# Optimization experiments

Hardware: AMD Instinct MI355X
Metric: run time of the kernel (lower is better)

The kernel has to match this reference:

```python
import jax, jax.numpy as jnp
import numpy as np

# token markers (module-level constants in the original repo)
PASS, MAP_EVT, STEP_EVT = 1, 2, 3
NUM_KEYS, NUM_VALUES, D_MODEL = 32, 32, 64
NUM_SYMBOLS = NUM_KEYS * 2  # 64
GRAPH_STEPS = 3
B, T = 4096, 256


def _mlp2(x, W1, b1, W2, b2):
    # Linear -> GELU (exact, matching torch nn.GELU default) -> Linear
    return jax.nn.gelu(x @ W1 + b1, approximate=False) @ W2 + b2


def setup_inputs() -> dict:
    key = jax.random.key(0)
    ks = jax.random.split(key, 32)
    d = D_MODEL

    def w(k, shape, scale=0.05):
        return jax.random.normal(k, shape, dtype=jnp.float32) * scale

    inp = {
        "evidence": jax.random.normal(ks[0], (B, T, d), dtype=jnp.float32),
        "event_marker": jax.random.randint(ks[1], (B, T), 0, 4, dtype=jnp.int32),
        "source_idx": jax.random.randint(ks[2], (B, T), 0, NUM_SYMBOLS, dtype=jnp.int32),
        "source_valid": jax.random.randint(ks[3], (B, T), 0, 2, dtype=jnp.int32),
        "target_symbol_idx": jax.random.randint(ks[4], (B, T), 0, NUM_SYMBOLS, dtype=jnp.int32),
        "target_symbol_valid": jax.random.randint(ks[5], (B, T), 0, 2, dtype=jnp.int32),
        "target_value_idx": jax.random.randint(ks[6], (B, T), 0, NUM_VALUES, dtype=jnp.int32),
        "target_value_valid": jax.random.randint(ks[7], (B, T), 0, 2, dtype=jnp.int32),
        "query_idx": jax.random.randint(ks[8], (B,), 0, NUM_SYMBOLS, dtype=jnp.int32),
        "query_valid": jax.random.randint(ks[9], (B,), 0, 2, dtype=jnp.int32),
        # embeddings
        "symbol_emb": w(ks[10], (NUM_SYMBOLS, d), 0.05),
        "value_emb": w(ks[11], (NUM_VALUES, d), 0.05),
        # map_gain MLP: Linear(d,d) GELU Linear(d,1)
        "mg_W1": w(ks[12], (d, d)), "mg_b1": jnp.zeros((d,), jnp.float32),
        "mg_W2": w(ks[13], (d, 1)), "mg_b2": jnp.zeros((1,), jnp.float32),
        # step_gain MLP
        "sg_W1": w(ks[14], (d, d)), "sg_b1": jnp.zeros((d,), jnp.float32),
        "sg_W2": w(ks[15], (d, 1)), "sg_b2": jnp.zeros((1,), jnp.float32),
        # slot_feedback MLP: Linear(2d,d) GELU Linear(d,d)
        "sf_W1": w(ks[16], (2 * d, d)), "sf_b1": jnp.zeros((d,), jnp.float32),
        "sf_W2": w(ks[17], (d, d)), "sf_b2": jnp.zeros((d,), jnp.float32),
        # output_head MLP: Linear(2d,d) GELU Linear(d,NUM_VALUES)
        "oh_W1": w(ks[18], (2 * d, d)), "oh_b1": jnp.zeros((d,), jnp.float32),
        "oh_W2": w(ks[19], (d, NUM_VALUES)), "oh_b2": jnp.zeros((NUM_VALUES,), jnp.float32),
    }
    return inp


def reference(evidence, event_marker, source_idx, source_valid, target_symbol_idx,
              target_symbol_valid, target_value_idx, target_value_valid,
              query_idx, query_valid, symbol_emb, value_emb,
              mg_W1, mg_b1, mg_W2, mg_b2, sg_W1, sg_b1, sg_W2, sg_b2,
              sf_W1, sf_b1, sf_W2, sf_b2, oh_W1, oh_b1, oh_W2, oh_b2):
    b, t = event_marker.shape
    dt = evidence.dtype

    # --- per-event gates (batched over all T events at once) ---
    map_gain = jax.nn.sigmoid(_mlp2(evidence, mg_W1, mg_b1, mg_W2, mg_b2))[..., 0]   # [B,T]
    step_gain = jax.nn.sigmoid(_mlp2(evidence, sg_W1, sg_b1, sg_W2, sg_b2))[..., 0]  # [B,T]

    src_v = source_valid.astype(bool)
    map_mask = ((event_marker == PASS) | (event_marker == MAP_EVT)) & src_v & target_value_valid.astype(bool)
    step_mask = (event_marker == STEP_EVT) & src_v & target_symbol_valid.astype(bool)

    src = jnp.clip(source_idx, 0, NUM_SYMBOLS - 1)
    tsym = jnp.clip(target_symbol_idx, 0, NUM_SYMBOLS - 1)
    tval = jnp.clip(target_value_idx, 0, NUM_VALUES - 1)

    # --- memory writes: sequential additive outer-product updates from a zero
    # init_state are order-independent, so they reduce to one scatter-add ---
    bb = jnp.broadcast_to(jnp.arange(b)[:, None], (b, t))
    map_memory = jnp.zeros((b, NUM_SYMBOLS, NUM_VALUES), dt).at[bb, src, tval].add(
        map_gain * map_mask.astype(dt))
    step_memory = jnp.zeros((b, NUM_SYMBOLS, NUM_SYMBOLS), dt).at[bb, src, tsym].add(
        step_gain * step_mask.astype(dt))

    # --- query_readout: 3-step graph walk ---
    walk = jax.nn.one_hot(jnp.clip(query_idx, 0, NUM_SYMBOLS - 1), NUM_SYMBOLS, dtype=dt)
    walk = walk * query_valid.astype(dt)[:, None]  # [B,S]

    acc_values = jnp.einsum('bs,bsv->bv', walk, map_memory)    # [B,V]
    acc_symbols = walk @ symbol_emb                             # [B,D]
    for _ in range(GRAPH_STEPS):
        walk = jnp.einsum('bs,bst->bt', walk, step_memory)
        acc_values = acc_values + jnp.einsum('bs,bsv->bv', walk, map_memory)
        acc_symbols = acc_symbols + walk @ symbol_emb

    graph_value_vec = acc_values @ value_emb                    # [B,D]
    graph_state = jnp.concatenate([acc_symbols, graph_value_vec], axis=-1)  # [B,2D]
    logits = _mlp2(graph_state, oh_W1, oh_b1, oh_W2, oh_b2)     # [B,NUM_VALUES]
    feedback = _mlp2(graph_state, sf_W1, sf_b1, sf_W2, sf_b2)   # [B,D]
    return logits, feedback
```

## Files before the change

### kernel.cpp

```cpp
#include <hip/hip_runtime.h>
#include <hip/hip_bf16.h>
#include <math.h>

#define T_LEN 256
#define NSYM 64
#define NVAL 32
#define DMOD 64

__device__ __forceinline__ float gelu_exact(float x) {
    return 0.5f * x * (1.0f + erff(x * 0.70710678118654752440f));
}
__device__ __forceinline__ float sigmoid_f(float x) {
    return 1.0f / (1.0f + expf(-x));
}

__global__ __launch_bounds__(256, 2) void k1_fused(
    const float* __restrict__ evidence,
    const int* __restrict__ event_marker,
    const int* __restrict__ source_idx,
    const int* __restrict__ source_valid,
    const int* __restrict__ tsym_idx,
    const int* __restrict__ tsym_valid,
    const int* __restrict__ tval_idx,
    const int* __restrict__ tval_valid,
    const int* __restrict__ query_idx,
    const int* __restrict__ query_valid,
    const float* __restrict__ symbol_emb,
    const float* __restrict__ value_emb,
    const float* __restrict__ mg_W1, const float* __restrict__ mg_b1,
    const float* __restrict__ mg_W2, const float* __restrict__ mg_b2,
    const float* __restrict__ sg_W1, const float* __restrict__ sg_b1,
    const float* __restrict__ sg_W2, const float* __restrict__ sg_b2,
    float* __restrict__ state_out)
{
    __shared__ int   s_src[T_LEN], s_tv[T_LEN], s_ts[T_LEN];
    __shared__ int   list_map[T_LEN], list_step[T_LEN];
    __shared__ int   cnts[2];
    __shared__ float mapM[NSYM * NVAL];
    __shared__ float stepM[NSYM * NSYM];
    __shared__ float W1s[64 * 64];
    __shared__ float W2s[64], b1s[64];
    __shared__ float b2s;
    __shared__ float X[64 * 65];
    __shared__ float wk[64], wk2[64], accv[32], accs[64];

    const int tid = threadIdx.x;
    const int b   = blockIdx.x;

    if (tid < 2) cnts[tid] = 0;
    for (int i = tid; i < NSYM * NVAL;  i += 256) mapM[i]  = 0.f;
    for (int i = tid; i < NSYM * NSYM;  i += 256) stepM[i] = 0.f;
    __syncthreads();

    {
        const int e  = b * T_LEN + tid;
        const int m  = event_marker[e];
        const int sv = source_valid[e];
        int src = source_idx[e]; src = src < 0 ? 0 : (src > 63 ? 63 : src);
        int ts  = tsym_idx[e];   ts  = ts  < 0 ? 0 : (ts  > 63 ? 63 : ts);
        int tv  = tval_idx[e];   tv  = tv  < 0 ? 0 : (tv  > 31 ? 31 : tv);
        s_src[tid] = src; s_ts[tid] = ts; s_tv[tid] = tv;
        const bool mm = ((m == 1) || (m == 2)) && (sv != 0) && (tval_valid[e] != 0);
        const bool sm = (m == 3) && (sv != 0) && (tsym_valid[e] != 0);
        if (mm) { int i = atomicAdd(&cnts[0], 1); list_map[i]  = tid; }
        if (sm) { int i = atomicAdd(&cnts[1], 1); list_step[i] = tid; }
    }
    __syncthreads();

    for (int type = 0; type < 2; ++type) {
        const float* W1g = (type == 0) ? mg_W1 : sg_W1;
        const float* W2g = (type == 0) ? mg_W2 : sg_W2;
        const float* b1g = (type == 0) ? mg_b1 : sg_b1;
        const float* b2g = (type == 0) ? mg_b2 : sg_b2;
        const int*   list = (type == 0) ? list_map : list_step;

        for (int i = tid; i < 4096; i += 256) W1s[i] = W1g[i];
        if (tid < 64) { W2s[tid] = W2g[tid]; b1s[tid] = b1g[tid]; }
        if (tid == 0) b2s = b2g[0];
        __syncthreads();

        const int cnt = cnts[type];
        for (int tile0 = 0; tile0 < cnt; tile0 += 64) {
            {
                const int r = tid >> 2, f4 = tid & 3;
                const int slot = tile0 + r;
                float* xd = &X[r * 65 + f4 * 16];
                if (slot < cnt) {
                    const int tev = list[slot];
                    const float* xg = evidence + ((size_t)(b * T_LEN + tev)) * 64 + f4 * 16;
                    #pragma unroll
                    for (int i = 0; i < 4; ++i) {
                        const float4 v = *reinterpret_cast<const float4*>(xg + i * 4);
                        xd[i * 4 + 0] = v.x; xd[i * 4 + 1] = v.y;
                        xd[i * 4 + 2] = v.z; xd[i * 4 + 3] = v.w;
                    }
                } else {
                    #pragma unroll
                    for (int i = 0; i < 16; ++i) xd[i] = 0.f;
                }
            }
            __syncthreads();

            float acc0[8], acc1[8];
            #pragma unroll
            for (int i = 0; i < 8; ++i) { acc0[i] = 0.f; acc1[i] = 0.f; }
            const int ep = tid >> 3, jo = tid & 7;
            const int j0 = jo * 8;
            const float* xp0 = &X[(ep * 2) * 65];
            const float* xp1 = &X[(ep * 2 + 1) * 65];
            #pragma unroll 8
            for (int k = 0; k < 64; ++k) {
                const float x0 = xp0[k], x1 = xp1[k];
                const float4 w0 = *reinterpret_cast<const float4*>(&W1s[k * 64 + j0]);
                const float4 w1 = *reinterpret_cast<const float4*>(&W1s[k * 64 + j0 + 4]);
                acc0[0] += x0 * w0.x; acc0[1] += x0 * w0.y;
                acc0[2] += x0 * w0.z; acc0[3] += x0 * w0.w;
                acc0[4] += x0 * w1.x; acc0[5] += x0 * w1.y;
                acc0[6] += x0 * w1.z; acc0[7] += x0 * w1.w;
                acc1[0] += x1 * w0.x; acc1[1] += x1 * w0.y;
                acc1[2] += x1 * w0.z; acc1[3] += x1 * w0.w;
                acc1[4] += x1 * w1.x; acc1[5] += x1 * w1.y;
                acc1[6] += x1 * w1.z; acc1[7] += x1 * w1.w;
            }
            float p0 = 0.f, p1 = 0.f;
            #pragma unroll
            for (int jj = 0; jj < 8; ++jj) {
                const float bb = b1s[j0 + jj], ww = W2s[j0 + jj];
                p0 += gelu_exact(acc0[jj] + bb) * ww;
                p1 += gelu_exact(acc1[jj] + bb) * ww;
            }
            p0 += __shfl_xor(p0, 1); p0 += __shfl_xor(p0, 2); p0 += __shfl_xor(p0, 4);
            p1 += __shfl_xor(p1, 1); p1 += __shfl_xor(p1, 2); p1 += __shfl_xor(p1, 4);

            if (jo == 0) {
                const float bb2 = b2s;
                const int slot0 = tile0 + ep * 2;
                if (slot0 < cnt) {
                    const int tev = list[slot0];
                    const float g = sigmoid_f(p0 + bb2);
                    if (type == 0) atomicAdd(&mapM[s_src[tev] * NVAL + s_tv[tev]], g);
                    else           atomicAdd(&stepM[s_src[tev] * NSYM + s_ts[tev]], g);
                }
                const int slot1 = slot0 + 1;
                if (slot1 < cnt) {
                    const int tev = list[slot1];
                    const float g = sigmoid_f(p1 + bb2);
                    if (type == 0) atomicAdd(&mapM[s_src[tev] * NVAL + s_tv[tev]], g);
                    else           atomicAdd(&stepM[s_src[tev] * NSYM + s_ts[tev]], g);
                }
            }
            __syncthreads();
        }
        __syncthreads();
    }

    {
        int q = query_idx[b]; q = q < 0 ? 0 : (q > 63 ? 63 : q);
        const float qv = (query_valid[b] != 0) ? 1.0f : 0.0f;
        if (tid < 64) wk[tid]  = (tid == q) ? qv : 0.f;
        if (tid < 32) accv[tid] = qv * mapM[q * NVAL + tid];
        if (tid < 64) accs[tid] = qv * symbol_emb[q * 64 + tid];
        __syncthreads();

        for (int st = 0; st < 3; ++st) {
            if (tid < 64) {
                float s = 0.f;
                #pragma unroll 8
                for (int s0 = 0; s0 < 64; ++s0) s += wk[s0] * stepM[s0 * NSYM + tid];
                wk2[tid] = s;
            }
            __syncthreads();
            if (tid < 64) wk[tid] = wk2[tid];
            __syncthreads();
            if (tid < 32) {
                float s = 0.f;
                #pragma unroll 8
                for (int s0 = 0; s0 < 64; ++s0) s += wk[s0] * mapM[s0 * NVAL + tid];
                accv[tid] += s;
            }
            if (tid < 64) {
                float s = 0.f;
                #pragma unroll 8
                for (int s0 = 0; s0 < 64; ++s0) s += wk[s0] * symbol_emb[s0 * 64 + tid];
                accs[tid] += s;
            }
            __syncthreads();
        }

        if (tid < 64) {
            float s = 0.f;
            #pragma unroll 8
            for (int v = 0; v < 32; ++v) s += accv[v] * value_emb[v * 64 + tid];
            state_out[(size_t)b * 128 + tid]      = accs[tid];
            state_out[(size_t)b * 128 + 64 + tid] = s;
        }
    }
}

__global__ __launch_bounds__(256) void k2_heads(
    const float* __restrict__ state,
    const float* __restrict__ sf_W1, const float* __restrict__ sf_b1,
    const float* __restrict__ sf_W2, const float* __restrict__ sf_b2,
    const float* __restrict__ oh_W1, const float* __restrict__ oh_b1,
    const float* __restrict__ oh_W2, const float* __restrict__ oh_b2,
    float* __restrict__ out, int B)
{
    __shared__ float h_oh[4][64];
    __shared__ float h_sf[4][64];
    const int tid = threadIdx.x;
    const int w = tid >> 6, j = tid & 63;
    const int b = blockIdx.x * 4 + w;
    {
        const float* st = state + (size_t)b * 128;
        float a_oh = oh_b1[j], a_sf = sf_b1[j];
        #pragma unroll 8
        for (int k = 0; k < 128; ++k) {
            const float sv = st[k];
            a_oh += sv * oh_W1[k * 64 + j];
            a_sf += sv * sf_W1[k * 64 + j];
        }
        h_oh[w][j] = gelu_exact(a_oh);
        h_sf[w][j] = gelu_exact(a_sf);
    }
    __syncthreads();

    for (int o = tid; o < 4 * 96; o += 256) {
        const int bb = o / 96, oo = o % 96;
        const int gb = blockIdx.x * 4 + bb;
        if (oo < 32) {
            float s = oh_b2[oo];
            #pragma unroll 8
            for (int jj = 0; jj < 64; ++jj) s += h_oh[bb][jj] * oh_W2[jj * 32 + oo];
            out[(size_t)gb * 32 + oo] = s;
        } else {
            const int dd = oo - 32;
            float s = sf_b2[dd];
            #pragma unroll 8
            for (int jj = 0; jj < 64; ++jj) s += h_sf[bb][jj] * sf_W2[jj * 64 + dd];
            out[(size_t)B * 32 + (size_t)gb * 64 + dd] = s;
        }
    }
}

extern "C" void kernel_launch(void* const* d_in, const int* in_sizes, int n_in,
                              void* d_out, int out_size, void* d_ws, size_t ws_size,
                              hipStream_t stream) {
    const float* evidence      = (const float*)d_in[0];
    const int*   event_marker  = (const int*)d_in[1];
    const int*   source_idx    = (const int*)d_in[2];
    const int*   source_valid  = (const int*)d_in[3];
    const int*   tsym_idx      = (const int*)d_in[4];
    const int*   tsym_valid    = (const int*)d_in[5];
    const int*   tval_idx      = (const int*)d_in[6];
    const int*   tval_valid    = (const int*)d_in[7];
    const int*   query_idx     = (const int*)d_in[8];
    const int*   query_valid   = (const int*)d_in[9];
    const float* symbol_emb    = (const float*)d_in[10];
    const float* value_emb     = (const float*)d_in[11];
    const float* mg_W1 = (const float*)d_in[12]; const float* mg_b1 = (const float*)d_in[13];
    const float* mg_W2 = (const float*)d_in[14]; const float* mg_b2 = (const float*)d_in[15];
    const float* sg_W1 = (const float*)d_in[16]; const float* sg_b1 = (const float*)d_in[17];
    const float* sg_W2 = (const float*)d_in[18]; const float* sg_b2 = (const float*)d_in[19];
    const float* sf_W1 = (const float*)d_in[20]; const float* sf_b1 = (const float*)d_in[21];
    const float* sf_W2 = (const float*)d_in[22]; const float* sf_b2 = (const float*)d_in[23];
    const float* oh_W1 = (const float*)d_in[24]; const float* oh_b1 = (const float*)d_in[25];
    const float* oh_W2 = (const float*)d_in[26]; const float* oh_b2 = (const float*)d_in[27];

    const int B = in_sizes[8];
    float* state = (float*)d_ws;

    k1_fused<<<B, 256, 0, stream>>>(
        evidence, event_marker, source_idx, source_valid,
        tsym_idx, tsym_valid, tval_idx, tval_valid,
        query_idx, query_valid, symbol_emb, value_emb,
        mg_W1, mg_b1, mg_W2, mg_b2, sg_W1, sg_b1, sg_W2, sg_b2,
        state);

    k2_heads<<<B / 4, 256, 0, stream>>>(
        state, sf_W1, sf_b1, sf_W2, sf_b2,
        oh_W1, oh_b1, oh_W2, oh_b2,
        (float*)d_out, B);
}
```

Before: 564.0 us.

## Hold MLP weights in registers and process one event per wavefront

Replaces the shared-memory tiled MLP (W1 and evidence staged in LDS, with block-wide syncs per tile) with a wavefront-per-event scheme. Each lane keeps one column of W1 in 64 registers, reads the event's evidence row directly from global memory as broadcast float4 loads, and reduces the second layer with wave shuffles. Dropping the W1, X and per-event index buffers shrinks LDS enough to raise the occupancy target to 4 blocks, and the per-tile barriers go away. The cost is heavy register pressure, redundant evidence loads across lanes, and only one output per wavefront per pass.

After: 556.6 us. No clear change (-1.3%).

```diff
diff --git a/kernel.cpp b/kernel.cpp
--- a/kernel.cpp
+++ b/kernel.cpp
@@ -5,7 +5,6 @@
 #define T_LEN 256
 #define NSYM 64
 #define NVAL 32
-#define DMOD 64
 
 __device__ __forceinline__ float gelu_exact(float x) {
     return 0.5f * x * (1.0f + erff(x * 0.70710678118654752440f));
@@ -14,7 +13,7 @@
     return 1.0f / (1.0f + expf(-x));
 }
 
-__global__ __launch_bounds__(256, 2) void k1_fused(
+__global__ __launch_bounds__(256, 4) void k1_fused(
     const float* __restrict__ evidence,
     const int* __restrict__ event_marker,
     const int* __restrict__ source_idx,
@@ -33,19 +32,17 @@
     const float* __restrict__ sg_W2, const float* __restrict__ sg_b2,
     float* __restrict__ state_out)
 {
-    __shared__ int   s_src[T_LEN], s_tv[T_LEN], s_ts[T_LEN];
-    __shared__ int   list_map[T_LEN], list_step[T_LEN];
+    __shared__ int   s_code[T_LEN];
+    __shared__ unsigned char l_map[T_LEN], l_step[T_LEN];
     __shared__ int   cnts[2];
     __shared__ float mapM[NSYM * NVAL];
     __shared__ float stepM[NSYM * NSYM];
-    __shared__ float W1s[64 * 64];
-    __shared__ float W2s[64], b1s[64];
-    __shared__ float b2s;
-    __shared__ float X[64 * 65];
     __shared__ float wk[64], wk2[64], accv[32], accs[64];
 
-    const int tid = threadIdx.x;
-    const int b   = blockIdx.x;
+    const int tid  = threadIdx.x;
+    const int b    = blockIdx.x;
+    const int lane = tid & 63;
+    const int wv   = tid >> 6;
 
     if (tid < 2) cnts[tid] = 0;
     for (int i = tid; i < NSYM * NVAL;  i += 256) mapM[i]  = 0.f;
@@ -59,100 +56,67 @@
         int src = source_idx[e]; src = src < 0 ? 0 : (src > 63 ? 63 : src);
         int ts  = tsym_idx[e];   ts  = ts  < 0 ? 0 : (ts  > 63 ? 63 : ts);
         int tv  = tval_idx[e];   tv  = tv  < 0 ? 0 : (tv  > 31 ? 31 : tv);
-        s_src[tid] = src; s_ts[tid] = ts; s_tv[tid] = tv;
+        s_code[tid] = src | (ts << 8) | (tv << 16);
         const bool mm = ((m == 1) || (m == 2)) && (sv != 0) && (tval_valid[e] != 0);
         const bool sm = (m == 3) && (sv != 0) && (tsym_valid[e] != 0);
-        if (mm) { int i = atomicAdd(&cnts[0], 1); list_map[i]  = tid; }
-        if (sm) { int i = atomicAdd(&cnts[1], 1); list_step[i] = tid; }
-    }
-    __syncthreads();
-
+        if (mm) { int i = atomicAdd(&cnts[0], 1); l_map[i]  = (unsigned char)tid; }
+        if (sm) { int i = atomicAdd(&cnts[1], 1); l_step[i] = (unsigned char)tid; }
+    }
+    __syncthreads();
+
+#define FMA4(v, kb) \
+    h0 = fmaf((v).x, w1c[(kb)+0], h0); h1 = fmaf((v).y, w1c[(kb)+1], h1); \
+    h2 = fmaf((v).z, w1c[(kb)+2], h2); h3 = fmaf((v).w, w1c[(kb)+3], h3);
+
+    #pragma unroll 1
     for (int type = 0; type < 2; ++type) {
-        const float* W1g = (type == 0) ? mg_W1 : sg_W1;
-        const float* W2g = (type == 0) ? mg_W2 : sg_W2;
-        const float* b1g = (type == 0) ? mg_b1 : sg_b1;
-        const float* b2g = (type == 0) ? mg_b2 : sg_b2;
-        const int*   list = (type == 0) ? list_map : list_step;
-
-        for (int i = tid; i < 4096; i += 256) W1s[i] = W1g[i];
-        if (tid < 64) { W2s[tid] = W2g[tid]; b1s[tid] = b1g[tid]; }
-        if (tid == 0) b2s = b2g[0];
-        __syncthreads();
-
         const int cnt = cnts[type];
-        for (int tile0 = 0; tile0 < cnt; tile0 += 64) {
-            {
-                const int r = tid >> 2, f4 = tid & 3;
-                const int slot = tile0 + r;
-                float* xd = &X[r * 65 + f4 * 16];
-                if (slot < cnt) {
-                    const int tev = list[slot];
-                    const float* xg = evidence + ((size_t)(b * T_LEN + tev)) * 64 + f4 * 16;
-                    #pragma unroll
-                    for (int i = 0; i < 4; ++i) {
-                        const float4 v = *reinterpret_cast<const float4*>(xg + i * 4);
-                        xd[i * 4 + 0] = v.x; xd[i * 4 + 1] = v.y;
-                        xd[i * 4 + 2] = v.z; xd[i * 4 + 3] = v.w;
-                    }
-                } else {
-                    #pragma unroll
-                    for (int i = 0; i < 16; ++i) xd[i] = 0.f;
-                }
-            }
-            __syncthreads();
-
-            float acc0[8], acc1[8];
-            #pragma unroll
-            for (int i = 0; i < 8; ++i) { acc0[i] = 0.f; acc1[i] = 0.f; }
-            const int ep = tid >> 3, jo = tid & 7;
-            const int j0 = jo * 8;
-            const float* xp0 = &X[(ep * 2) * 65];
-            const float* xp1 = &X[(ep * 2 + 1) * 65];
-            #pragma unroll 8
-            for (int k = 0; k < 64; ++k) {
-                const float x0 = xp0[k], x1 = xp1[k];
-                const float4 w0 = *reinterpret_cast<const float4*>(&W1s[k * 64 + j0]);
-                const float4 w1 = *reinterpret_cast<const float4*>(&W1s[k * 64 + j0 + 4]);
-                acc0[0] += x0 * w0.x; acc0[1] += x0 * w0.y;
-                acc0[2] += x0 * w0.z; acc0[3] += x0 * w0.w;
-                acc0[4] += x0 * w1.x; acc0[5] += x0 * w1.y;
-                acc0[6] += x0 * w1.z; acc0[7] += x0 * w1.w;
-                acc1[0] += x1 * w0.x; acc1[1] += x1 * w0.y;
-                acc1[2] += x1 * w0.z; acc1[3] += x1 * w0.w;
-                acc1[4] += x1 * w1.x; acc1[5] += x1 * w1.y;
-                acc1[6] += x1 * w1.z; acc1[7] += x1 * w1.w;
-            }
-            float p0 = 0.f, p1 = 0.f;
-            #pragma unroll
-            for (int jj = 0; jj < 8; ++jj) {
-                const float bb = b1s[j0 + jj], ww = W2s[j0 + jj];
-                p0 += gelu_exact(acc0[jj] + bb) * ww;
-                p1 += gelu_exact(acc1[jj] + bb) * ww;
-            }
-            p0 += __shfl_xor(p0, 1); p0 += __shfl_xor(p0, 2); p0 += __shfl_xor(p0, 4);
-            p1 += __shfl_xor(p1, 1); p1 += __shfl_xor(p1, 2); p1 += __shfl_xor(p1, 4);
-
-            if (jo == 0) {
-                const float bb2 = b2s;
-                const int slot0 = tile0 + ep * 2;
-                if (slot0 < cnt) {
-                    const int tev = list[slot0];
-                    const float g = sigmoid_f(p0 + bb2);
-                    if (type == 0) atomicAdd(&mapM[s_src[tev] * NVAL + s_tv[tev]], g);
-                    else           atomicAdd(&stepM[s_src[tev] * NSYM + s_ts[tev]], g);
-                }
-                const int slot1 = slot0 + 1;
-                if (slot1 < cnt) {
-                    const int tev = list[slot1];
-                    const float g = sigmoid_f(p1 + bb2);
-                    if (type == 0) atomicAdd(&mapM[s_src[tev] * NVAL + s_tv[tev]], g);
-                    else           atomicAdd(&stepM[s_src[tev] * NSYM + s_ts[tev]], g);
-                }
-            }
-            __syncthreads();
-        }
-        __syncthreads();
-    }
+        if (cnt == 0) continue;
+        const float* __restrict__ W1g = (type == 0) ? mg_W1 : sg_W1;
+        const float* __restrict__ W2g = (type == 0) ? mg_W2 : sg_W2;
+        const float* __restrict__ b1g = (type == 0) ? mg_b1 : sg_b1;
+        const float* __restrict__ b2g = (type == 0) ? mg_b2 : sg_b2;
+        const unsigned char* list = (type == 0) ? l_map : l_step;
+
+        float w1c[64];
+        #pragma unroll
+        for (int k = 0; k < 64; ++k) w1c[k] = W1g[k * 64 + lane];
+        const float b1j = b1g[lane];
+        const float w2j = W2g[lane];
+        const float b2v = b2g[0];
+
+        for (int i = wv; i < cnt; i += 4) {
+            const int t = list[i];
+            const float4* __restrict__ xr =
+                (const float4*)(evidence + ((size_t)b * T_LEN + t) * 64);
+            float4 a0 = xr[0], a1 = xr[1], a2 = xr[2],  a3 = xr[3];
+            float4 c0 = xr[4], c1 = xr[5], c2 = xr[6],  c3 = xr[7];
+            float h0 = b1j, h1 = 0.f, h2 = 0.f, h3 = 0.f;
+            FMA4(a0, 0)  FMA4(a1, 4)  FMA4(a2, 8)  FMA4(a3, 12)
+            a0 = xr[8]; a1 = xr[9]; a2 = xr[10]; a3 = xr[11];
+            FMA4(c0, 16) FMA4(c1, 20) FMA4(c2, 24) FMA4(c3, 28)
+            c0 = xr[12]; c1 = xr[13]; c2 = xr[14]; c3 = xr[15];
+            FMA4(a0, 32) FMA4(a1, 36) FMA4(a2, 40) FMA4(a3, 44)
+            FMA4(c0, 48) FMA4(c1, 52) FMA4(c2, 56) FMA4(c3, 60)
+
+            const float hj = (h0 + h1) + (h2 + h3);
+            float gj = gelu_exact(hj) * w2j;
+            gj += __shfl_xor(gj, 1);  gj += __shfl_xor(gj, 2);
+            gj += __shfl_xor(gj, 4);  gj += __shfl_xor(gj, 8);
+            gj += __shfl_xor(gj, 16); gj += __shfl_xor(gj, 32);
+
+            if (lane == 0) {
+                const float g = sigmoid_f(gj + b2v);
+                const int code = s_code[t];
+                if (type == 0)
+                    atomicAdd(&mapM[(code & 63) * NVAL + ((code >> 16) & 31)], g);
+                else
+                    atomicAdd(&stepM[(code & 63) * NSYM + ((code >> 8) & 63)], g);
+            }
+        }
+    }
+#undef FMA4
+    __syncthreads();
 
     {
         int q = query_idx[b]; q = q < 0 ? 0 : (q > 63 ? 63 : q);
```
